# Kernel tuning notes

Hardware: AMD Instinct MI355X
Metric: run time of the kernel (lower is better)

The kernel has to match this reference:

```python
import jax, jax.numpy as jnp
import numpy as np

C = 1024
H = 16
D = C // H

def setup_inputs() -> dict:
    key = jax.random.key(0)
    ks = jax.random.split(key, 12)
    s = 1.0 / np.sqrt(C)
    inp = {
        "Q": jax.random.normal(ks[0], (2, 1024, C), jnp.float32),
        "K_in": jax.random.normal(ks[1], (2, 4096, C), jnp.float32),
        "V_in": jax.random.normal(ks[2], (2, 4096, C), jnp.float32),
        "V_bias": jax.random.normal(ks[3], (2, 4096), jnp.float32),
        "Wq_w": jax.random.uniform(ks[4], (C, C), jnp.float32, -s, s),
        "Wq_b": jax.random.uniform(ks[5], (C,), jnp.float32, -s, s),
        "Wk_w": jax.random.uniform(ks[6], (C, C), jnp.float32, -s, s),
        "Wk_b": jax.random.uniform(ks[7], (C,), jnp.float32, -s, s),
        "Wv_w": jax.random.uniform(ks[8], (C, C), jnp.float32, -s, s),
        "Wv_b": jax.random.uniform(ks[9], (C,), jnp.float32, -s, s),
        "Wo_w": jax.random.uniform(ks[10], (C, C), jnp.float32, -s, s),
        "Wo_b": jax.random.uniform(ks[11], (C,), jnp.float32, -s, s),
    }
    return inp

def reference(Q, K_in, V_in, V_bias, Wq_w, Wq_b, Wk_w, Wk_b, Wv_w, Wv_b, Wo_w, Wo_b):
    B, Lq, _ = Q.shape
    Lk = K_in.shape[1]
    # linear projections (torch Linear: x @ W.T + b), split heads -> [B,H,L,D]
    q = (Q @ Wq_w.T + Wq_b).reshape(B, Lq, H, D).transpose(0, 2, 1, 3)
    k = (K_in @ Wk_w.T + Wk_b).reshape(B, Lk, H, D).transpose(0, 2, 1, 3)
    v = (V_in @ Wv_w.T + Wv_b).reshape(B, Lk, H, D).transpose(0, 2, 1, 3)
    scale = 1.0 / np.sqrt(D).astype(np.float32)
    logits = jnp.einsum("bhqd,bhkd->bhqk", q, k) * scale
    logits = logits + V_bias[:, None, None, :]  # per-key additive bias
    attn = jax.nn.softmax(logits, axis=-1)      # dropout p=0.0 (eval)
    out = jnp.einsum("bhqk,bhkd->bhqd", attn, v)
    out = out.transpose(0, 2, 1, 3).reshape(B, Lq, C)
    return out @ Wo_w.T + Wo_b
```

## Files before the change

### kernel.cpp

```cpp
#include <hip/hip_runtime.h>


typedef __attribute__((ext_vector_type(8))) __bf16 bf16x8;
typedef __attribute__((ext_vector_type(4))) float f32x4;
typedef __attribute__((ext_vector_type(16))) float f32x16;

#define LOG2E 1.44269504f
#define MFIX 24.0f

__device__ __forceinline__ unsigned short f2bf(float f) {
  union { float f; unsigned u; } v; v.f = f;
  unsigned r = v.u + 0x7fffu + ((v.u >> 16) & 1u);
  return (unsigned short)(r >> 16);
}
__device__ __forceinline__ unsigned short f2h(float x) {
  _Float16 h = (_Float16)x;
  return __builtin_bit_cast(unsigned short, h);
}
__device__ __forceinline__ float h2f(unsigned short u) {
  return (float)__builtin_bit_cast(_Float16, u);
}

__device__ __forceinline__ f32x4 mfma16(bf16x8 a, bf16x8 b, f32x4 c) {
  return __builtin_amdgcn_mfma_f32_16x16x32_bf16(a, b, c, 0, 0, 0);
}
__device__ __forceinline__ f32x16 mfma32(bf16x8 a, bf16x8 b, f32x16 c) {
  return __builtin_amdgcn_mfma_f32_32x32x16_bf16(a, b, c, 0, 0, 0);
}

__device__ __forceinline__ unsigned pk2(float lo, float hi) {
  unsigned short a = __builtin_bit_cast(unsigned short, (__bf16)lo);
  unsigned short b = __builtin_bit_cast(unsigned short, (__bf16)hi);
  return (unsigned)a | ((unsigned)b << 16);
}

template <typename T>
__device__ __forceinline__ void gload16(const T* g, T* l) {
  __builtin_amdgcn_global_load_lds(
      (const __attribute__((address_space(1))) void*)g,
      (__attribute__((address_space(3))) void*)l, 16, 0, 0);
}

struct CvtJob { const float* src; unsigned short* dst; int n4; };
struct CvtArgs { CvtJob j[6]; };

__global__ __launch_bounds__(256) void cvt_kernel(CvtArgs a) {
  const CvtJob jb = a.j[blockIdx.y];
  const float4* s = (const float4*)jb.src;
  unsigned short* d = jb.dst;
  const int stride = gridDim.x * blockDim.x;
  for (int i = blockIdx.x * blockDim.x + threadIdx.x; i < jb.n4; i += stride) {
    float4 f = s[i];
    ushort4 u;
    u.x = f2bf(f.x); u.y = f2bf(f.y); u.z = f2bf(f.z); u.w = f2bf(f.w);
    ((ushort4*)d)[i] = u;
  }
}

__global__ __launch_bounds__(256) void prep_kb(const float* __restrict__ Vb,
                                               unsigned* __restrict__ kb) {
  const int i = blockIdx.x * 256 + threadIdx.x;
  const float x = Vb[i] * LOG2E;
  const unsigned short h = f2bf(x);
  union { unsigned u; float f; } hf; hf.u = (unsigned)h << 16;
  const unsigned short lo = f2bf(x - hf.f);
  kb[i] = (unsigned)h | ((unsigned)lo << 16);
}

struct ProjSeg {
  const unsigned short* A; const unsigned short* W; const float* bias;
  void* out; int mode; int Llog2; float oscale;
};
struct ProjArgs { ProjSeg s[2]; int start1; };

__global__ __launch_bounds__(256, 2) void proj_gemm(ProjArgs pa) {
  constexpr int K = 1024;
  __shared__ unsigned short Alds[2][128][64];
  __shared__ unsigned short Blds[2][128][64];

  const int bid = blockIdx.x;
  const int si = (bid >= pa.start1) ? 1 : 0;
  const ProjSeg sg = pa.s[si];
  const int local = bid - (si ? pa.start1 : 0);
  const int xcd = local & 7, jj = local >> 3;
  const int m0 = ((jj >> 3) * 8 + xcd) * 128;
  const int n0 = (jj & 7) * 128;

  const int tid = threadIdx.x;
  const int wid = tid >> 6, l = tid & 63;
  const int wr = wid >> 1, wc = wid & 1;
  const int lg = l >> 4, lm = l & 15;

  const int srow = wid * 8 + (l >> 3);
  const int scol = ((l & 7) ^ (l >> 3)) * 8;
  const unsigned short* aS = sg.A + (long)(m0 + srow) * K + scol;
  const unsigned short* bS = sg.W + (long)(n0 + srow) * K + scol;

  f32x4 acc[4][4] = {};

  auto issue = [&](int kt, int buf) {
#pragma unroll
    for (int c = 0; c < 4; ++c) {
      gload16(aS + ((long)c * 32) * K + kt * 64,
              &Alds[buf][c * 32 + wid * 8][0]);
      gload16(bS + ((long)c * 32) * K + kt * 64,
              &Blds[buf][c * 32 + wid * 8][0]);
    }
  };

  issue(0, 0);
  issue(1, 1);

  for (int t = 0; t < 16; ++t) {
    if (t < 15) asm volatile("s_waitcnt vmcnt(8)" ::: "memory");
    else        asm volatile("s_waitcnt vmcnt(0)" ::: "memory");
    __builtin_amdgcn_sched_barrier(0);
    __builtin_amdgcn_s_barrier();
    const int buf = t & 1;

#pragma unroll
    for (int kc = 0; kc < 2; ++kc) {
      bf16x8 af[4], bf[4];
#pragma unroll
      for (int i = 0; i < 4; ++i) {
        const int so = ((kc * 4 + lg) ^ (lm & 7)) * 8;
        af[i] = *(const bf16x8*)&Alds[buf][wr * 64 + i * 16 + lm][so];
        bf[i] = *(const bf16x8*)&Blds[buf][wc * 64 + i * 16 + lm][so];
      }
      __builtin_amdgcn_s_setprio(1);
      if (sg.mode == 1) {
#pragma unroll
        for (int i = 0; i < 4; ++i)
#pragma unroll
          for (int j = 0; j < 4; ++j)
            acc[i][j] = mfma16(bf[i], af[j], acc[i][j]);
      } else {
#pragma unroll
        for (int i = 0; i < 4; ++i)
#pragma unroll
          for (int j = 0; j < 4; ++j)
            acc[i][j] = mfma16(af[i], bf[j], acc[i][j]);
      }
      __builtin_amdgcn_s_setprio(0);
    }

    __builtin_amdgcn_s_barrier();
    if (t + 2 < 16) issue(t + 2, buf);
  }

  const int rr = lg * 4;
  if (sg.mode == 0) {
    const int Lmask = (1 << sg.Llog2) - 1;
    unsigned short* out = (unsigned short*)sg.out;
#pragma unroll
    for (int j = 0; j < 4; ++j) {
      const int n = n0 + wc * 64 + j * 16 + lm;
      const float bv = sg.bias[n];
      const int h = n >> 6, d = n & 63;
#pragma unroll
      for (int i = 0; i < 4; ++i)
#pragma unroll
        for (int r = 0; r < 4; ++r) {
          const int m = m0 + wr * 64 + i * 16 + rr + r;
          const int b = m >> sg.Llog2, li = m & Lmask;
          const long o = (((long)(b * 16 + h) << sg.Llog2) + li) * 64 + d;
          out[o] = f2bf((acc[i][j][r] + bv) * sg.oscale);
        }
    }
  } else if (sg.mode == 1) {
    unsigned short* out = (unsigned short*)sg.out;
#pragma unroll
    for (int i = 0; i < 4; ++i)
#pragma unroll
      for (int r = 0; r < 4; ++r) {
        const int n = n0 + wc * 64 + i * 16 + rr + r;
        const float bv = sg.bias[n];
        const int h = n >> 6, d = n & 63;
#pragma unroll
        for (int j = 0; j < 4; ++j) {
          const int m = m0 + wr * 64 + j * 16 + lm;
          const int b = m >> 12, lk = m & 4095;
          const long o = ((long)((b * 16 + h) * 64 + d)) * 4096 + lk;
          out[o] = f2bf(acc[i][j][r] + bv);
        }
      }
  } else {
    float* out = (float*)sg.out;
#pragma unroll
    for (int j = 0; j < 4; ++j) {
      const int n = n0 + wc * 64 + j * 16 + lm;
      const float bv = sg.bias[n];
#pragma unroll
      for (int i = 0; i < 4; ++i)
#pragma unroll
        for (int r = 0; r < 4; ++r) {
          const int m = m0 + wr * 64 + i * 16 + rr + r;
          out[(long)m * 1024 + n] = acc[i][j][r] + bv;
        }
    }
  }
}

__global__ __launch_bounds__(256, 2) void attn64(
    const unsigned short* __restrict__ qh, const unsigned short* __restrict__ kh,
    const unsigned short* __restrict__ vT, const unsigned* __restrict__ kb,
    unsigned short* __restrict__ Oh, float* __restrict__ ml) {
  __shared__ unsigned short Klds[2][64][64];
  __shared__ unsigned short Vlds[2][64][64];

  const int tid = threadIdx.x;
  const int wid = tid >> 6, lane = tid & 63;
  const int lq = lane & 31, hi = lane >> 5;
  const int bh = blockIdx.x, qb = blockIdx.y, sp = blockIdx.z;
  const int b = bh >> 4;
  const int qA = qb * 256 + wid * 64 + lq;
  const int kt0 = sp * 16;

  bf16x8 qrA[4], qrB[4];
  {
    const unsigned short* qp = qh + ((long)bh * 1024 + qA) * 64 + hi * 8;
#pragma unroll
    for (int dc = 0; dc < 4; ++dc) {
      qrA[dc] = *(const bf16x8*)(qp + dc * 16);
      qrB[dc] = *(const bf16x8*)(qp + 32 * 64 + dc * 16);
    }
  }

  union uv { uint4 u; bf16x8 v; };
  uv bq; bq.u = make_uint4(hi ? 0u : 0x3F803F80u, 0u, 0u, 0u);

  auto swap23 = [](int r) { return (r & 0x33) | ((r & 4) << 1) | ((r & 8) >> 1); };
  const int r0 = wid * 16 + (lane >> 3), r1 = r0 + 8;
  const int s0 = ((lane & 7) ^ (r0 & 7)) * 8;
  const int s1 = ((lane & 7) ^ (r1 & 7)) * 8;
  const unsigned short* kg0 =
      kh + ((long)bh * 4096 + kt0 * 64 + swap23(r0)) * 64 + s0;
  const unsigned short* kg1 =
      kh + ((long)bh * 4096 + kt0 * 64 + swap23(r1)) * 64 + s1;
  const unsigned short* vg0 = vT + ((long)bh * 64 + r0) * 4096 + kt0 * 64 + s0;
  const unsigned short* vg1 = vT + ((long)bh * 64 + r1) * 4096 + kt0 * 64 + s1;
  const unsigned* kbp = kb + b * 4096 + kt0 * 64;
  const int kbkey = swap23(lq);

  auto issue = [&](int t, int buf) {
    gload16(kg0 + (long)t * 4096, &Klds[buf][wid * 16][0]);
    gload16(kg1 + (long)t * 4096, &Klds[buf][wid * 16 + 8][0]);
    gload16(vg0 + t * 64, &Vlds[buf][wid * 16][0]);
    gload16(vg1 + t * 64, &Vlds[buf][wid * 16 + 8][0]);
  };
  issue(0, 0);

  const int rsw = lq & 7;
  float lA = 0.f, lB = 0.f;
  f32x16 oaA0 = {}, oaA1 = {}, oaB0 = {}, oaB1 = {};
  uv puA[4], puB[4];

  auto softmax = [&](const f32x16& sx0, const f32x16& sx1, float& lreg,
                     uv* pu) {
    float p[32];
#pragma unroll
    for (int r = 0; r < 16; ++r) {
      p[r] = __builtin_amdgcn_exp2f(sx0[r] - MFIX);
      p[16 + r] = __builtin_amdgcn_exp2f(sx1[r] - MFIX);
    }
    float s16[16];
#pragma unroll
    for (int i = 0; i < 16; ++i) s16[i] = p[i] + p[i + 16];
#pragma unroll
    for (int s = 8; s > 0; s >>= 1)
#pragma unroll
      for (int i = 0; i < 8; ++i)
        if (i < s) s16[i] += s16[i + s];
    lreg += s16[0] + __shfl_xor(s16[0], 32);
#pragma unroll
    for (int kc = 0; kc < 4; ++kc)
      pu[kc].u = make_uint4(pk2(p[kc * 8 + 0], p[kc * 8 + 1]),
                            pk2(p[kc * 8 + 2], p[kc * 8 + 3]),
                            pk2(p[kc * 8 + 4], p[kc * 8 + 5]),
                            pk2(p[kc * 8 + 6], p[kc * 8 + 7]));
  };

  for (int t = 0; t < 16; ++t) {
    const int buf = t & 1;
    __syncthreads();
    if (t + 1 < 16) issue(t + 1, buf ^ 1);

    uv ka0, ka1;
    ka0.u = make_uint4(hi ? 0u : kbp[t * 64 + kbkey], 0u, 0u, 0u);
    ka1.u = make_uint4(hi ? 0u : kbp[t * 64 + 32 + kbkey], 0u, 0u, 0u);

    bf16x8 kf0[4], kf1[4];
#pragma unroll
    for (int dc = 0; dc < 4; ++dc) {
      const int so = ((dc * 2 + hi) ^ rsw) * 8;
      kf0[dc] = *(const bf16x8*)&Klds[buf][lq][so];
      kf1[dc] = *(const bf16x8*)&Klds[buf][32 + lq][so];
    }

    f32x16 sa0 = {}, sa1 = {}, sb0 = {}, sb1 = {};
    __builtin_amdgcn_s_setprio(1);
#pragma unroll
    for (int dc = 0; dc < 4; ++dc) {
      sa0 = mfma32(kf0[dc], qrA[dc], sa0);
      sa1 = mfma32(kf1[dc], qrA[dc], sa1);
      sb0 = mfma32(kf0[dc], qrB[dc], sb0);
      sb1 = mfma32(kf1[dc], qrB[dc], sb1);
    }
    sa0 = mfma32(ka0.v, bq.v, sa0);
    sa1 = mfma32(ka1.v, bq.v, sa1);
    sb0 = mfma32(ka0.v, bq.v, sb0);
    sb1 = mfma32(ka1.v, bq.v, sb1);
    __builtin_amdgcn_s_setprio(0);

    softmax(sa0, sa1, lA, puA);

    bf16x8 vf0[4], vf1[4];
#pragma unroll
    for (int kc = 0; kc < 4; ++kc) {
      const int so = ((kc * 2 + hi) ^ rsw) * 8;
      vf0[kc] = *(const bf16x8*)&Vlds[buf][lq][so];
      vf1[kc] = *(const bf16x8*)&Vlds[buf][32 + lq][so];
    }

    __builtin_amdgcn_s_setprio(1);
#pragma unroll
    for (int kc = 0; kc < 4; ++kc) {
      oaA0 = mfma32(vf0[kc], puA[kc].v, oaA0);
      oaA1 = mfma32(vf1[kc], puA[kc].v, oaA1);
    }
    __builtin_amdgcn_s_setprio(0);

    softmax(sb0, sb1, lB, puB);

    __builtin_amdgcn_s_setprio(1);
#pragma unroll
    for (int kc = 0; kc < 4; ++kc) {
      oaB0 = mfma32(vf0[kc], puB[kc].v, oaB0);
      oaB1 = mfma32(vf1[kc], puB[kc].v, oaB1);
    }
    __builtin_amdgcn_s_setprio(0);
  }

  const float invA = 1.0f / lA, invB = 1.0f / lB;
  unsigned short* obA = Oh + (((long)sp * 32 + bh) * 1024 + qA) * 64 + hi * 4;
  unsigned short* obB = obA + 32 * 64;
#pragma unroll
  for (int g = 0; g < 4; ++g) {
    ushort4 u;
    u.x = f2h(oaA0[g * 4 + 0] * invA); u.y = f2h(oaA0[g * 4 + 1] * invA);
    u.z = f2h(oaA0[g * 4 + 2] * invA); u.w = f2h(oaA0[g * 4 + 3] * invA);
    *(ushort4*)(obA + g * 8) = u;
    u.x = f2h(oaA1[g * 4 + 0] * invA); u.y = f2h(oaA1[g * 4 + 1] * invA);
    u.z = f2h(oaA1[g * 4 + 2] * invA); u.w = f2h(oaA1[g * 4 + 3] * invA);
    *(ushort4*)(obA + 32 + g * 8) = u;
    u.x = f2h(oaB0[g * 4 + 0] * invB); u.y = f2h(oaB0[g * 4 + 1] * invB);
    u.z = f2h(oaB0[g * 4 + 2] * invB); u.w = f2h(oaB0[g * 4 + 3] * invB);
    *(ushort4*)(obB + g * 8) = u;
    u.x = f2h(oaB1[g * 4 + 0] * invB); u.y = f2h(oaB1[g * 4 + 1] * invB);
    u.z = f2h(oaB1[g * 4 + 2] * invB); u.w = f2h(oaB1[g * 4 + 3] * invB);
    *(ushort4*)(obB + 32 + g * 8) = u;
  }
  if (hi == 0) {
    *(float2*)(ml + (((long)sp * 32 + bh) * 1024 + qA) * 2) =
        make_float2(MFIX, lA);
    *(float2*)(ml + (((long)sp * 32 + bh) * 1024 + qA + 32) * 2) =
        make_float2(MFIX, lB);
  }
}

__global__ __launch_bounds__(256) void combine4(
    const unsigned short* __restrict__ Oh, const float* __restrict__ ml,
    unsigned short* __restrict__ ao) {
  const int idx = blockIdx.x * 256 + threadIdx.x;
  const int bh = idx >> 10, q = idx & 1023;
  const int b = bh >> 4, h = bh & 15;
  float m[4], l[4];
#pragma unroll
  for (int i = 0; i < 4; ++i) {
    float2 t = *(const float2*)(ml + ((long)i * 32768 + idx) * 2);
    m[i] = t.x; l[i] = t.y;
  }
  const float mm = fmaxf(fmaxf(m[0], m[1]), fmaxf(m[2], m[3]));
  float w[4], wsum = 0.f;
#pragma unroll
  for (int i = 0; i < 4; ++i) {
    w[i] = l[i] * __builtin_amdgcn_exp2f(m[i] - mm);
    wsum += w[i];
  }
  const float inv = 1.0f / wsum;
#pragma unroll
  for (int i = 0; i < 4; ++i) w[i] *= inv;

  unsigned short* op = ao + ((long)b * 1024 + q) * 1024 + h * 64;
#pragma unroll
  for (int blk = 0; blk < 8; ++blk) {
    float acc[8] = {};
#pragma unroll
    for (int i = 0; i < 4; ++i) {
      uint4 u = *(const uint4*)(Oh + ((long)i * 32768 + idx) * 64 + blk * 8);
      const unsigned short* hs = (const unsigned short*)&u;
#pragma unroll
      for (int j = 0; j < 8; ++j) acc[j] += w[i] * h2f(hs[j]);
    }
    ushort4 o0, o1;
    o0.x = f2bf(acc[0]); o0.y = f2bf(acc[1]);
    o0.z = f2bf(acc[2]); o0.w = f2bf(acc[3]);
    o1.x = f2bf(acc[4]); o1.y = f2bf(acc[5]);
    o1.z = f2bf(acc[6]); o1.w = f2bf(acc[7]);
    *(ushort4*)(op + blk * 8) = o0;
    *(ushort4*)(op + blk * 8 + 4) = o1;
  }
}

extern "C" void kernel_launch(void* const* d_in, const int* in_sizes, int n_in,
                              void* d_out, int out_size, void* d_ws,
                              size_t ws_size, hipStream_t stream) {
  const float* Q = (const float*)d_in[0];
  const float* K_in = (const float*)d_in[1];
  const float* V_in = (const float*)d_in[2];
  const float* V_bias = (const float*)d_in[3];
  const float* Wq_w = (const float*)d_in[4];
  const float* Wq_b = (const float*)d_in[5];
  const float* Wk_w = (const float*)d_in[6];
  const float* Wk_b = (const float*)d_in[7];
  const float* Wv_w = (const float*)d_in[8];
  const float* Wv_b = (const float*)d_in[9];
  const float* Wo_w = (const float*)d_in[10];
  const float* Wo_b = (const float*)d_in[11];

  char* ws = (char*)d_ws;
  unsigned short* Wqb = (unsigned short*)(ws + (0l << 20));
  float* mlp = (float*)(ws + (0l << 20));
  unsigned short* Wkb = (unsigned short*)(ws + (2l << 20));
  unsigned short* Wvb = (unsigned short*)(ws + (4l << 20));
  unsigned short* Wob = (unsigned short*)(ws + (6l << 20));
  unsigned short* qhp = (unsigned short*)(ws + (8l << 20));
  unsigned short* khp = (unsigned short*)(ws + (12l << 20));
  unsigned short* vTp = (unsigned short*)(ws + (28l << 20));
  unsigned short* Qbf = (unsigned short*)(ws + (44l << 20));
  unsigned short* Kbf = (unsigned short*)(ws + (48l << 20));
  unsigned short* Vbf = (unsigned short*)(ws + (48l << 20));
  unsigned short* Ohp = (unsigned short*)(ws + (44l << 20));
  unsigned short* aop = (unsigned short*)(ws + (60l << 20));
  unsigned* kbp = (unsigned*)(ws + (64l << 20));

  CvtArgs c1;
  c1.j[0] = CvtJob{Wq_w, Wqb, 262144};
  c1.j[1] = CvtJob{Wk_w, Wkb, 262144};
  c1.j[2] = CvtJob{Wv_w, Wvb, 262144};
  c1.j[3] = CvtJob{Wo_w, Wob, 262144};
  c1.j[4] = CvtJob{Q, Qbf, 524288};
  c1.j[5] = CvtJob{K_in, Kbf, 2097152};
  cvt_kernel<<<dim3(512, 6), 256, 0, stream>>>(c1);
  prep_kb<<<32, 256, 0, stream>>>(V_bias, kbp);

  ProjArgs pA;
  pA.s[0] = ProjSeg{Kbf, Wkb, Wk_b, khp, 0, 12, 1.0f};
  pA.s[1] = ProjSeg{Qbf, Wqb, Wq_b, qhp, 0, 10, 0.125f * LOG2E};
  pA.start1 = 512;
  proj_gemm<<<640, 256, 0, stream>>>(pA);

  CvtArgs c2;
  c2.j[0] = CvtJob{V_in, Vbf, 2097152};
  c2.j[1] = c2.j[0]; c2.j[2] = c2.j[0];
  c2.j[3] = c2.j[0]; c2.j[4] = c2.j[0]; c2.j[5] = c2.j[0];
  cvt_kernel<<<dim3(512, 1), 256, 0, stream>>>(c2);

  ProjArgs pB;
  pB.s[0] = ProjSeg{Vbf, Wvb, Wv_b, vTp, 1, 12, 1.0f};
  pB.s[1] = pB.s[0];
  pB.start1 = 1 << 30;
  proj_gemm<<<512, 256, 0, stream>>>(pB);

  attn64<<<dim3(32, 4, 4), 256, 0, stream>>>(qhp, khp, vTp, kbp, Ohp, mlp);
  combine4<<<128, 256, 0, stream>>>(Ohp, mlp, aop);

  ProjArgs pO;
  pO.s[0] = ProjSeg{aop, Wob, Wo_b, d_out, 2, 0, 1.0f};
  pO.s[1] = pO.s[0];
  pO.start1 = 1 << 30;
  proj_gemm<<<128, 256, 0, stream>>>(pO);
}
```

Before: 172.0 us.

## Raise attention split-K to 8 when workspace allows, deepen K/V prefetch

When the workspace is large enough, the attention kernel splits the key range eight ways instead of four, doubling the grid to 1024 blocks. The combine kernel becomes generic over the split count. It drops the max-rescale, since every split uses a fixed softmax offset. The K/V loads are now double-issued two tiles ahead, with explicit vmcnt waits and barriers in place of a single syncthreads, and the key-bias loads are prefetched into registers. The changes aim at better occupancy and latency hiding, at the cost of more partial-output traffic and a larger combine step.

```diff
diff --git a/kernel.cpp b/kernel.cpp
--- a/kernel.cpp
+++ b/kernel.cpp
@@ -201,10 +201,10 @@
   }
 }
 
-__global__ __launch_bounds__(256, 2) void attn64(
+__global__ __launch_bounds__(256, 4) void attn64(
     const unsigned short* __restrict__ qh, const unsigned short* __restrict__ kh,
     const unsigned short* __restrict__ vT, const unsigned* __restrict__ kb,
-    unsigned short* __restrict__ Oh, float* __restrict__ ml) {
+    unsigned short* __restrict__ Oh, float* __restrict__ ml, int nt) {
   __shared__ unsigned short Klds[2][64][64];
   __shared__ unsigned short Vlds[2][64][64];
 
@@ -214,7 +214,7 @@
   const int bh = blockIdx.x, qb = blockIdx.y, sp = blockIdx.z;
   const int b = bh >> 4;
   const int qA = qb * 256 + wid * 64 + lq;
-  const int kt0 = sp * 16;
+  const int kt0 = sp * nt;
 
   bf16x8 qrA[4], qrB[4];
   {
@@ -242,13 +242,17 @@
   const unsigned* kbp = kb + b * 4096 + kt0 * 64;
   const int kbkey = swap23(lq);
 
+  unsigned kbw0[2], kbw1[2];
   auto issue = [&](int t, int buf) {
     gload16(kg0 + (long)t * 4096, &Klds[buf][wid * 16][0]);
     gload16(kg1 + (long)t * 4096, &Klds[buf][wid * 16 + 8][0]);
     gload16(vg0 + t * 64, &Vlds[buf][wid * 16][0]);
     gload16(vg1 + t * 64, &Vlds[buf][wid * 16 + 8][0]);
+    kbw0[buf] = kbp[t * 64 + kbkey];
+    kbw1[buf] = kbp[t * 64 + 32 + kbkey];
   };
   issue(0, 0);
+  issue(1, 1);
 
   const int rsw = lq & 7;
   float lA = 0.f, lB = 0.f;
@@ -280,14 +284,16 @@
                             pk2(p[kc * 8 + 6], p[kc * 8 + 7]));
   };
 
-  for (int t = 0; t < 16; ++t) {
+  for (int t = 0; t < nt; ++t) {
     const int buf = t & 1;
-    __syncthreads();
-    if (t + 1 < 16) issue(t + 1, buf ^ 1);
+    if (t < nt - 1) asm volatile("s_waitcnt vmcnt(6)" ::: "memory");
+    else            asm volatile("s_waitcnt vmcnt(0)" ::: "memory");
+    __builtin_amdgcn_sched_barrier(0);
+    __builtin_amdgcn_s_barrier();
 
     uv ka0, ka1;
-    ka0.u = make_uint4(hi ? 0u : kbp[t * 64 + kbkey], 0u, 0u, 0u);
-    ka1.u = make_uint4(hi ? 0u : kbp[t * 64 + 32 + kbkey], 0u, 0u, 0u);
+    ka0.u = make_uint4(hi ? 0u : kbw0[buf], 0u, 0u, 0u);
+    ka1.u = make_uint4(hi ? 0u : kbw1[buf], 0u, 0u, 0u);
 
     bf16x8 kf0[4], kf1[4];
 #pragma unroll
@@ -339,6 +345,9 @@
       oaB1 = mfma32(vf1[kc], puB[kc].v, oaB1);
     }
     __builtin_amdgcn_s_setprio(0);
+
+    __builtin_amdgcn_s_barrier();
+    if (t + 2 < nt) issue(t + 2, buf);
   }
 
   const float invA = 1.0f / lA, invB = 1.0f / lB;
@@ -368,35 +377,25 @@
   }
 }
 
-__global__ __launch_bounds__(256) void combine4(
+__global__ __launch_bounds__(256) void combineN(
     const unsigned short* __restrict__ Oh, const float* __restrict__ ml,
-    unsigned short* __restrict__ ao) {
+    unsigned short* __restrict__ ao, int NS) {
   const int idx = blockIdx.x * 256 + threadIdx.x;
   const int bh = idx >> 10, q = idx & 1023;
   const int b = bh >> 4, h = bh & 15;
-  float m[4], l[4];
-#pragma unroll
-  for (int i = 0; i < 4; ++i) {
-    float2 t = *(const float2*)(ml + ((long)i * 32768 + idx) * 2);
-    m[i] = t.x; l[i] = t.y;
-  }
-  const float mm = fmaxf(fmaxf(m[0], m[1]), fmaxf(m[2], m[3]));
-  float w[4], wsum = 0.f;
-#pragma unroll
-  for (int i = 0; i < 4; ++i) {
-    w[i] = l[i] * __builtin_amdgcn_exp2f(m[i] - mm);
+  float w[8], wsum = 0.f;
+  for (int i = 0; i < NS; ++i) {
+    w[i] = ml[((long)i * 32768 + idx) * 2 + 1];
     wsum += w[i];
   }
   const float inv = 1.0f / wsum;
-#pragma unroll
-  for (int i = 0; i < 4; ++i) w[i] *= inv;
+  for (int i = 0; i < NS; ++i) w[i] *= inv;
 
   unsigned short* op = ao + ((long)b * 1024 + q) * 1024 + h * 64;
 #pragma unroll
   for (int blk = 0; blk < 8; ++blk) {
     float acc[8] = {};
-#pragma unroll
-    for (int i = 0; i < 4; ++i) {
+    for (int i = 0; i < NS; ++i) {
       uint4 u = *(const uint4*)(Oh + ((long)i * 32768 + idx) * 64 + blk * 8);
       const unsigned short* hs = (const unsigned short*)&u;
 #pragma unroll
@@ -420,13 +419,16 @@
   const float* V_in = (const float*)d_in[2];
   const float* V_bias = (const float*)d_in[3];
   const float* Wq_w = (const float*)d_in[4];
+  const float* Wk_w = (const float*)d_in[6];
+  const float* Wv_w = (const float*)d_in[8];
+  const float* Wo_w = (const float*)d_in[10];
   const float* Wq_b = (const float*)d_in[5];
-  const float* Wk_w = (const float*)d_in[6];
   const float* Wk_b = (const float*)d_in[7];
-  const float* Wv_w = (const float*)d_in[8];
   const float* Wv_b = (const float*)d_in[9];
-  const float* Wo_w = (const float*)d_in[10];
   const float* Wo_b = (const float*)d_in[11];
+
+  const int NS = (ws_size >= ((81ull << 20))) ? 8 : 4;
+  const int nt = 64 / NS;
 
   char* ws = (char*)d_ws;
   unsigned short* Wqb = (unsigned short*)(ws + (0l << 20));
@@ -441,8 +443,8 @@
   unsigned short* Kbf = (unsigned short*)(ws + (48l << 20));
   unsigned short* Vbf = (unsigned short*)(ws + (48l << 20));
   unsigned short* Ohp = (unsigned short*)(ws + (44l << 20));
-  unsigned short* aop = (unsigned short*)(ws + (60l << 20));
-  unsigned* kbp = (unsigned*)(ws + (64l << 20));
+  unsigned short* aop = (unsigned short*)(ws + ((44l + 4 * NS) << 20));
+  unsigned* kbp = (unsigned*)(ws + ((48l + 4 * NS) << 20));
 
   CvtArgs c1;
   c1.j[0] = CvtJob{Wq_w, Wqb, 262144};
@@ -472,8 +474,8 @@
   pB.start1 = 1 << 30;
   proj_gemm<<<512, 256, 0, stream>>>(pB);
 
-  attn64<<<dim3(32, 4, 4), 256, 0, stream>>>(qhp, khp, vTp, kbp, Ohp, mlp);
-  combine4<<<128, 256, 0, stream>>>(Ohp, mlp, aop);
+  attn64<<<dim3(32, 4, NS), 256, 0, stream>>>(qhp, khp, vTp, kbp, Ohp, mlp, nt);
+  combineN<<<128, 256, 0, stream>>>(Ohp, mlp, aop, NS);
 
   ProjArgs pO;
   pO.s[0] = ProjSeg{aop, Wob, Wo_b, d_out, 2, 0, 1.0f};
```

New measurement: 473.8 us (median of 4 runs). +175.4%, slower.
